# Kernel tuning notes

Hardware: AMD Instinct MI355X
Metric: run time of the kernel (lower is better)

## Reference

```python
import jax, jax.numpy as jnp
import numpy as np

PY_SIZES = [256, 64]
BASE = 256


def _resize_bilinear_ac(x, out):
    # NCHW bilinear resize, align_corners=True (matches F.interpolate(..., align_corners=True))
    def interp(x, axis, in_size):
        pos = jnp.arange(out, dtype=jnp.float32) * (in_size - 1) / (out - 1)
        lo = jnp.floor(pos).astype(jnp.int32)
        hi = jnp.minimum(lo + 1, in_size - 1)
        w = (pos - lo.astype(jnp.float32)).astype(x.dtype)
        shp = [1] * x.ndim
        shp[axis] = out
        w = w.reshape(shp)
        return jnp.take(x, lo, axis=axis) * (1 - w) + jnp.take(x, hi, axis=axis) * w
    x = interp(x, 2, x.shape[2])
    x = interp(x, 3, x.shape[3])
    return x


def _area_pool(x, f):
    # F.interpolate(mode='area') for integer downscale factor f == average pooling
    B, C, H, W = x.shape
    return x.reshape(B, C, H // f, f, W // f, f).mean(axis=(3, 5))


def _nearest_up_int(x, out):
    # F.interpolate(mode='nearest'): src = floor(dst * in/out)
    h = x.shape[2]
    idx = (jnp.arange(out) * h) // out
    return x[:, :, idx][:, :, :, idx]


def _buffers(B):
    grids, lin_ids, img_ids = [], [], []
    prev = 0
    for S in PY_SIZES:
        d = jnp.arange(S, dtype=jnp.float32) + 0.5
        gy, gx = jnp.meshgrid(d, d, indexing='ij')
        grids.append(jnp.broadcast_to(jnp.stack([gy, gx], -1)[None, None], (B, 1, S, S, 2)))
        lin_ids.append(jnp.arange(B * S * S, dtype=jnp.int32).reshape(B, 1, S, S) + prev)
        prev += B * S * S
        img_ids.append(jnp.broadcast_to(jnp.arange(B, dtype=jnp.float32)[:, None, None, None], (B, 1, S, S)))
    return grids, lin_ids, img_ids


def setup_inputs():
    key = jax.random.key(0)
    k1, k2 = jax.random.split(key)
    b_edges = (jax.random.uniform(k1, (64, 1, 512, 512)) < 0.08).astype(jnp.float32)
    sobel = jax.random.normal(k2, (64, 2, 512, 512), dtype=jnp.float32)
    return {"b_edges": b_edges, "sobel": sobel}


def reference(b_edges, sobel):
    B = b_edges.shape[0]
    grids, lin_ids, img_ids = _buffers(B)
    # resize post-Canny maps to base pyramid level
    e0 = jnp.clip(_resize_bilinear_ac(b_edges, BASE), 0, 1)
    s0 = _resize_bilinear_ac(sobel, BASE)
    py = [(e0, s0)]
    for S in PY_SIZES[1:]:
        f = BASE // S
        py.append((_area_pool(e0, f), _area_pool(s0, f)))
    p_lin, my_lin, centers, norms, sizes, imgid = [], [], [], [], [], []
    for i, (e, s) in enumerate(py):
        S = e.shape[2]
        idx = jnp.nonzero((e != 0).reshape(-1))[0]  # stream compaction of edge pixels
        if i + 1 < len(py):
            pl = _nearest_up_int(lin_ids[i + 1], S).reshape(-1)[idx]
        else:
            pl = lin_ids[i].reshape(-1)[idx]
        rat = BASE / S
        p_lin.append(pl)
        my_lin.append(lin_ids[i].reshape(-1)[idx])
        centers.append(grids[i].reshape(-1, 2)[idx] * rat)
        norms.append(jnp.transpose(s, (0, 2, 3, 1)).reshape(-1, 2)[idx])
        sizes.append(jnp.full(idx.shape, rat, dtype=jnp.float32))
        imgid.append(img_ids[i].reshape(-1)[idx])
    p_lin = jnp.concatenate(p_lin)
    my_lin = jnp.concatenate(my_lin)
    centers = jnp.concatenate(centers)
    norms = jnp.concatenate(norms)
    sizes = jnp.concatenate(sizes)
    imgid = jnp.concatenate(imgid)
    # parent scatter: linid -> row of that string, then gather by parent linid
    rowids = jnp.arange(my_lin.shape[0], dtype=jnp.int32)
    table = jnp.zeros(int(p_lin.max()) + 1, dtype=jnp.int32).at[my_lin].set(rowids)
    p_rowids = table[p_lin]
    norms = norms / jnp.linalg.norm(norms, axis=1, keepdims=True)
    # cross([nx,ny,0],[0,0,1]) = (ny,-nx,0)
    rt = jnp.stack([norms[:, 1], -norms[:, 0]], -1) * (sizes[:, None] / 2)
    locs_lf = centers + rt
    locs_rt = centers - rt
    return locs_lf, locs_rt, norms, sizes, centers, imgid, p_rowids, my_lin
```

## Files before the change

### kernel.cpp

```cpp
#include <hip/hip_runtime.h>
#include <math.h>


typedef unsigned long long u64;
#define OFFSET1 4194304

__global__ __launch_bounds__(256) void prepE_kernel(const float* __restrict__ E,
                                                    unsigned short* __restrict__ pred16,
                                                    u64* __restrict__ mask1,
                                                    int* __restrict__ counts0,
                                                    int* __restrict__ counts1) {
    int lane = threadIdx.x & 63;
    int g = blockIdx.x * 4 + (threadIdx.x >> 6);
    int b = g >> 6, R = g & 63;

    const float* Ep = E + b * 262144 + (8 * R) * 512 + 8 * lane;
    float4 L[8], H[8];
    #pragma unroll
    for (int k = 0; k < 8; ++k) {
        L[k] = *(const float4*)(Ep + k * 512);
        H[k] = *(const float4*)(Ep + k * 512 + 4);
    }

    float wx[4], cwx[4];
    #pragma unroll
    for (int j = 0; j < 4; ++j) {
        int xi = 4 * lane + j;
        wx[j] = (float)(xi * 511) / 255.0f - (float)(8 * lane + 2 * j);
        cwx[j] = 1.0f - wx[j];
    }

    unsigned pred = 0;
    int rc = 0;
    #pragma unroll
    for (int r = 0; r < 4; ++r) {
        int y = 4 * R + r;
        float wy = (float)(y * 511) / 255.0f - (float)(2 * y);
        float cwy = 1.0f - wy;
        float4 lo = L[2 * r], loh = H[2 * r];
        float4 hi = L[2 * r + 1], hih = H[2 * r + 1];
        float e0 = (lo.x*cwy + hi.x*wy)*cwx[0] + (lo.y*cwy + hi.y*wy)*wx[0];
        float e1 = (lo.z*cwy + hi.z*wy)*cwx[1] + (lo.w*cwy + hi.w*wy)*wx[1];
        float e2 = (loh.x*cwy + hih.x*wy)*cwx[2] + (loh.y*cwy + hih.y*wy)*wx[2];
        float e3 = (loh.z*cwy + hih.z*wy)*cwx[3] + (loh.w*cwy + hih.w*wy)*wx[3];
        bool p0 = (e0 != 0.0f), p1 = (e1 != 0.0f), p2 = (e2 != 0.0f), p3 = (e3 != 0.0f);
        pred |= (p0?1u:0u) << (4*r+0);
        pred |= (p1?1u:0u) << (4*r+1);
        pred |= (p2?1u:0u) << (4*r+2);
        pred |= (p3?1u:0u) << (4*r+3);
        u64 b0 = __ballot(p0), b1 = __ballot(p1), b2 = __ballot(p2), b3 = __ballot(p3);
        rc += __popcll(b0) + __popcll(b1) + __popcll(b2) + __popcll(b3);
    }
    u64 m1 = __ballot(pred != 0);
    pred16[g * 64 + lane] = (unsigned short)pred;
    if (lane == 0) {
        counts0[g] = rc;
        counts1[g] = __popcll(m1);
        mask1[g] = m1;
    }
}

__global__ __launch_bounds__(1024) void scan_kernel(const int* __restrict__ counts0,
                                                    int* __restrict__ offs0,
                                                    const int* __restrict__ counts1,
                                                    int* __restrict__ offs1,
                                                    int* __restrict__ totals) {
    __shared__ int wsum[16];
    int tid = threadIdx.x, lane = tid & 63, wave = tid >> 6;

    int carry = 0;
    for (int base = 0; base < 4096; base += 1024) {
        int v = counts0[base + tid];
        int inc = v;
        #pragma unroll
        for (int d = 1; d < 64; d <<= 1) {
            int t = __shfl_up(inc, (unsigned)d, 64);
            if (lane >= d) inc += t;
        }
        if (lane == 63) wsum[wave] = inc;
        __syncthreads();
        int wbase = 0;
        for (int i = 0; i < wave; ++i) wbase += wsum[i];
        int tot = 0;
        #pragma unroll
        for (int i = 0; i < 16; ++i) tot += wsum[i];
        offs0[base + tid] = carry + wbase + inc - v;
        carry += tot;
        __syncthreads();
    }
    if (tid == 0) totals[0] = carry;

    int carry1 = 0;
    for (int base = 0; base < 4096; base += 1024) {
        int v = counts1[base + tid];
        int inc = v;
        #pragma unroll
        for (int d = 1; d < 64; d <<= 1) {
            int t = __shfl_up(inc, (unsigned)d, 64);
            if (lane >= d) inc += t;
        }
        if (lane == 63) wsum[wave] = inc;
        __syncthreads();
        int wbase = 0;
        for (int i = 0; i < wave; ++i) wbase += wsum[i];
        int tot = 0;
        #pragma unroll
        for (int i = 0; i < 16; ++i) tot += wsum[i];
        offs1[base + tid] = carry1 + wbase + inc - v;
        carry1 += tot;
        __syncthreads();
    }
    if (tid == 0) totals[1] = carry1;
}

__device__ __forceinline__ void write_row(float* __restrict__ out, int N, int row,
                                          float cy, float cx, float s0v, float s1v,
                                          float half, float sz, float imgid,
                                          float prow, float mylin) {
    float len = sqrtf(s0v * s0v + s1v * s1v);
    float n0 = s0v / len, n1 = s1v / len;
    float rt0 = n1 * half, rt1 = -n0 * half;
    ((float2*)out)[row]           = make_float2(cy + rt0, cx + rt1);
    ((float2*)(out + 2 * N))[row] = make_float2(cy - rt0, cx - rt1);
    ((float2*)(out + 4 * N))[row] = make_float2(n0, n1);
    out[6 * N + row] = sz;
    ((float2*)(out + 7 * N))[row] = make_float2(cy, cx);
    out[9 * N + row] = imgid;
    out[10 * N + row] = prow;
    out[11 * N + row] = mylin;
}

__global__ __launch_bounds__(256) void prepS_kernel(const float* __restrict__ S,
                                                    const unsigned short* __restrict__ pred16,
                                                    const u64* __restrict__ mask1,
                                                    const int* __restrict__ offs0,
                                                    const int* __restrict__ offs1,
                                                    const int* __restrict__ totals,
                                                    float* __restrict__ out, int N) {
    int lane = threadIdx.x & 63;
    int g = blockIdx.x * 4 + (threadIdx.x >> 6);
    int bimg = g >> 6, R = g & 63;

    u64 m1 = mask1[g];
    if (m1 == 0ull) return;
    unsigned pred = pred16[g * 64 + lane];
    int base0 = offs0[g];
    int prow = totals[0] + offs1[g] + __popcll(m1 & ((1ull << lane) - 1ull));

    float wx[4], cwx[4];
    #pragma unroll
    for (int j = 0; j < 4; ++j) {
        int xi = 4 * lane + j;
        wx[j] = (float)(xi * 511) / 255.0f - (float)(8 * lane + 2 * j);
        cwx[j] = 1.0f - wx[j];
    }

    const float* Sa = S + (size_t)(2 * bimg) * 262144 + (8 * R) * 512 + 8 * lane;
    const float* Sq = Sa + 262144;

    float acc0 = 0.0f, acc1 = 0.0f;
    int rc = 0;
    #pragma unroll
    for (int h = 0; h < 2; ++h) {
        float4 A[4], Ax[4], Q[4], Qx[4];
        #pragma unroll
        for (int k = 0; k < 4; ++k) {
            const float* pa = Sa + (4 * h + k) * 512;
            A[k]  = *(const float4*)pa;
            Ax[k] = *(const float4*)(pa + 4);
            const float* pq = Sq + (4 * h + k) * 512;
            Q[k]  = *(const float4*)pq;
            Qx[k] = *(const float4*)(pq + 4);
        }
        #pragma unroll
        for (int rr = 0; rr < 2; ++rr) {
            int r = 2 * h + rr;
            int y = 4 * R + r;
            float wy = (float)(y * 511) / 255.0f - (float)(2 * y);
            float cwy = 1.0f - wy;
            float4 lo = A[2*rr], loh = Ax[2*rr], hi = A[2*rr+1], hih = Ax[2*rr+1];
            float4 ql = Q[2*rr], qlh = Qx[2*rr], qh = Q[2*rr+1], qhh = Qx[2*rr+1];
            float va[4], vb[4];
            va[0] = (lo.x*cwy + hi.x*wy)*cwx[0] + (lo.y*cwy + hi.y*wy)*wx[0];
            va[1] = (lo.z*cwy + hi.z*wy)*cwx[1] + (lo.w*cwy + hi.w*wy)*wx[1];
            va[2] = (loh.x*cwy + hih.x*wy)*cwx[2] + (loh.y*cwy + hih.y*wy)*wx[2];
            va[3] = (loh.z*cwy + hih.z*wy)*cwx[3] + (loh.w*cwy + hih.w*wy)*wx[3];
            vb[0] = (ql.x*cwy + qh.x*wy)*cwx[0] + (ql.y*cwy + qh.y*wy)*wx[0];
            vb[1] = (ql.z*cwy + qh.z*wy)*cwx[1] + (ql.w*cwy + qh.w*wy)*wx[1];
            vb[2] = (qlh.x*cwy + qhh.x*wy)*cwx[2] + (qlh.y*cwy + qhh.y*wy)*wx[2];
            vb[3] = (qlh.z*cwy + qhh.z*wy)*cwx[3] + (qlh.w*cwy + qhh.w*wy)*wx[3];
            acc0 += va[0] + va[1] + va[2] + va[3];
            acc1 += vb[0] + vb[1] + vb[2] + vb[3];

            unsigned pr = (pred >> (4 * r)) & 0xF;
            u64 b0 = __ballot(pr & 1);
            u64 b1 = __ballot(pr & 2);
            u64 b2 = __ballot(pr & 4);
            u64 b3 = __ballot(pr & 8);
            u64 ltm = (1ull << lane) - 1ull;
            int pre = __popcll(b0 & ltm) + __popcll(b1 & ltm) +
                      __popcll(b2 & ltm) + __popcll(b3 & ltm);
            int rbase = base0 + rc + pre;
            int own = 0;
            #pragma unroll
            for (int j = 0; j < 4; ++j) {
                if (pr & (1u << j)) {
                    int row = rbase + own;
                    own++;
                    int x = 4 * lane + j;
                    float cy = (float)y + 0.5f, cx = (float)x + 0.5f;
                    write_row(out, N, row, cy, cx, va[j], vb[j], 0.5f, 1.0f,
                              (float)bimg, (float)prow,
                              (float)((bimg << 16) + (y << 8) + x));
                }
            }
            rc += __popcll(b0) + __popcll(b1) + __popcll(b2) + __popcll(b3);
        }
    }

    if (pred != 0) {
        float v0 = acc0 * (1.0f / 16.0f), v1 = acc1 * (1.0f / 16.0f);
        float cy = ((float)R + 0.5f) * 4.0f, cx = ((float)lane + 0.5f) * 4.0f;
        write_row(out, N, prow, cy, cx, v0, v1, 2.0f, 4.0f, (float)bimg,
                  (float)prow, (float)(OFFSET1 + g * 64 + lane));
    }
}

extern "C" void kernel_launch(void* const* d_in, const int* in_sizes, int n_in,
                              void* d_out, int out_size, void* d_ws, size_t ws_size,
                              hipStream_t stream) {
    const float* E = (const float*)d_in[0];
    const float* S = (const float*)d_in[1];
    float* out = (float*)d_out;
    int N = out_size / 12;

    char* ws = (char*)d_ws;
    int* counts0 = (int*)(ws + 0);
    int* offs0   = (int*)(ws + 16384);
    int* counts1 = (int*)(ws + 32768);
    int* offs1   = (int*)(ws + 49152);
    int* totals  = (int*)(ws + 65536);
    u64* mask1   = (u64*)(ws + 65600);
    unsigned short* pred16 = (unsigned short*)(ws + 98368);

    prepE_kernel<<<1024, 256, 0, stream>>>(E, pred16, mask1, counts0, counts1);
    scan_kernel<<<1, 1024, 0, stream>>>(counts0, offs0, counts1, offs1, totals);
    prepS_kernel<<<1024, 256, 0, stream>>>(S, pred16, mask1, offs0, offs1,
                                           totals, out, N);
}
```

Measured before the change: 75.86 us.

## Split sobel resize kernel into half-row waves plus a level-1 finish kernel

```diff
diff --git a/kernel.cpp b/kernel.cpp
--- a/kernel.cpp
+++ b/kernel.cpp
@@ -130,20 +130,22 @@
     out[11 * N + row] = mylin;
 }
 
-__global__ __launch_bounds__(256) void prepS_kernel(const float* __restrict__ S,
-                                                    const unsigned short* __restrict__ pred16,
-                                                    const u64* __restrict__ mask1,
-                                                    const int* __restrict__ offs0,
-                                                    const int* __restrict__ offs1,
-                                                    const int* __restrict__ totals,
-                                                    float* __restrict__ out, int N) {
-    int lane = threadIdx.x & 63;
-    int g = blockIdx.x * 4 + (threadIdx.x >> 6);
+__global__ __launch_bounds__(256) void prepSa_kernel(const float* __restrict__ S,
+                                                     const unsigned short* __restrict__ pred16,
+                                                     const u64* __restrict__ mask1,
+                                                     const int* __restrict__ offs0,
+                                                     const int* __restrict__ offs1,
+                                                     const int* __restrict__ totals,
+                                                     float2* __restrict__ part,
+                                                     float* __restrict__ out, int N) {
+    int tid = threadIdx.x;
+    int lane = tid & 63;
+    int gh = blockIdx.x * 4 + (tid >> 6);
+    int g = gh >> 1, h = gh & 1;
     int bimg = g >> 6, R = g & 63;
 
+    unsigned pred = pred16[g * 64 + lane];
     u64 m1 = mask1[g];
-    if (m1 == 0ull) return;
-    unsigned pred = pred16[g * 64 + lane];
     int base0 = offs0[g];
     int prow = totals[0] + offs1[g] + __popcll(m1 & ((1ull << lane) - 1ull));
 
@@ -155,75 +157,95 @@
         cwx[j] = 1.0f - wx[j];
     }
 
-    const float* Sa = S + (size_t)(2 * bimg) * 262144 + (8 * R) * 512 + 8 * lane;
+    const float* Sa = S + (size_t)(2 * bimg) * 262144 + (8 * R + 4 * h) * 512 + 8 * lane;
     const float* Sq = Sa + 262144;
+    float4 A[4], Ax[4], Q[4], Qx[4];
+    #pragma unroll
+    for (int k = 0; k < 4; ++k) {
+        A[k]  = *(const float4*)(Sa + k * 512);
+        Ax[k] = *(const float4*)(Sa + k * 512 + 4);
+        Q[k]  = *(const float4*)(Sq + k * 512);
+        Qx[k] = *(const float4*)(Sq + k * 512 + 4);
+    }
+
+    int rc = 0;
+    if (h) {
+        #pragma unroll
+        for (int r = 0; r < 2; ++r) {
+            unsigned pr = (pred >> (4 * r)) & 0xF;
+            rc += __popcll(__ballot((pr & 1) != 0)) + __popcll(__ballot((pr & 2) != 0)) +
+                  __popcll(__ballot((pr & 4) != 0)) + __popcll(__ballot((pr & 8) != 0));
+        }
+    }
 
     float acc0 = 0.0f, acc1 = 0.0f;
-    int rc = 0;
-    #pragma unroll
-    for (int h = 0; h < 2; ++h) {
-        float4 A[4], Ax[4], Q[4], Qx[4];
-        #pragma unroll
-        for (int k = 0; k < 4; ++k) {
-            const float* pa = Sa + (4 * h + k) * 512;
-            A[k]  = *(const float4*)pa;
-            Ax[k] = *(const float4*)(pa + 4);
-            const float* pq = Sq + (4 * h + k) * 512;
-            Q[k]  = *(const float4*)pq;
-            Qx[k] = *(const float4*)(pq + 4);
-        }
-        #pragma unroll
-        for (int rr = 0; rr < 2; ++rr) {
-            int r = 2 * h + rr;
-            int y = 4 * R + r;
-            float wy = (float)(y * 511) / 255.0f - (float)(2 * y);
-            float cwy = 1.0f - wy;
-            float4 lo = A[2*rr], loh = Ax[2*rr], hi = A[2*rr+1], hih = Ax[2*rr+1];
-            float4 ql = Q[2*rr], qlh = Qx[2*rr], qh = Q[2*rr+1], qhh = Qx[2*rr+1];
-            float va[4], vb[4];
-            va[0] = (lo.x*cwy + hi.x*wy)*cwx[0] + (lo.y*cwy + hi.y*wy)*wx[0];
-            va[1] = (lo.z*cwy + hi.z*wy)*cwx[1] + (lo.w*cwy + hi.w*wy)*wx[1];
-            va[2] = (loh.x*cwy + hih.x*wy)*cwx[2] + (loh.y*cwy + hih.y*wy)*wx[2];
-            va[3] = (loh.z*cwy + hih.z*wy)*cwx[3] + (loh.w*cwy + hih.w*wy)*wx[3];
-            vb[0] = (ql.x*cwy + qh.x*wy)*cwx[0] + (ql.y*cwy + qh.y*wy)*wx[0];
-            vb[1] = (ql.z*cwy + qh.z*wy)*cwx[1] + (ql.w*cwy + qh.w*wy)*wx[1];
-            vb[2] = (qlh.x*cwy + qhh.x*wy)*cwx[2] + (qlh.y*cwy + qhh.y*wy)*wx[2];
-            vb[3] = (qlh.z*cwy + qhh.z*wy)*cwx[3] + (qlh.w*cwy + qhh.w*wy)*wx[3];
-            acc0 += va[0] + va[1] + va[2] + va[3];
-            acc1 += vb[0] + vb[1] + vb[2] + vb[3];
-
-            unsigned pr = (pred >> (4 * r)) & 0xF;
-            u64 b0 = __ballot(pr & 1);
-            u64 b1 = __ballot(pr & 2);
-            u64 b2 = __ballot(pr & 4);
-            u64 b3 = __ballot(pr & 8);
-            u64 ltm = (1ull << lane) - 1ull;
-            int pre = __popcll(b0 & ltm) + __popcll(b1 & ltm) +
-                      __popcll(b2 & ltm) + __popcll(b3 & ltm);
-            int rbase = base0 + rc + pre;
-            int own = 0;
-            #pragma unroll
-            for (int j = 0; j < 4; ++j) {
-                if (pr & (1u << j)) {
-                    int row = rbase + own;
-                    own++;
-                    int x = 4 * lane + j;
-                    float cy = (float)y + 0.5f, cx = (float)x + 0.5f;
-                    write_row(out, N, row, cy, cx, va[j], vb[j], 0.5f, 1.0f,
-                              (float)bimg, (float)prow,
-                              (float)((bimg << 16) + (y << 8) + x));
-                }
+    #pragma unroll
+    for (int rr = 0; rr < 2; ++rr) {
+        int r = 2 * h + rr;
+        int y = 4 * R + r;
+        float wy = (float)(y * 511) / 255.0f - (float)(2 * y);
+        float cwy = 1.0f - wy;
+        float4 lo = A[2*rr], loh = Ax[2*rr], hi = A[2*rr+1], hih = Ax[2*rr+1];
+        float4 ql = Q[2*rr], qlh = Qx[2*rr], qh = Q[2*rr+1], qhh = Qx[2*rr+1];
+        float va[4], vb[4];
+        va[0] = (lo.x*cwy + hi.x*wy)*cwx[0] + (lo.y*cwy + hi.y*wy)*wx[0];
+        va[1] = (lo.z*cwy + hi.z*wy)*cwx[1] + (lo.w*cwy + hi.w*wy)*wx[1];
+        va[2] = (loh.x*cwy + hih.x*wy)*cwx[2] + (loh.y*cwy + hih.y*wy)*wx[2];
+        va[3] = (loh.z*cwy + hih.z*wy)*cwx[3] + (loh.w*cwy + hih.w*wy)*wx[3];
+        vb[0] = (ql.x*cwy + qh.x*wy)*cwx[0] + (ql.y*cwy + qh.y*wy)*wx[0];
+        vb[1] = (ql.z*cwy + qh.z*wy)*cwx[1] + (ql.w*cwy + qh.w*wy)*wx[1];
+        vb[2] = (qlh.x*cwy + qhh.x*wy)*cwx[2] + (qlh.y*cwy + qhh.y*wy)*wx[2];
+        vb[3] = (qlh.z*cwy + qhh.z*wy)*cwx[3] + (qlh.w*cwy + qhh.w*wy)*wx[3];
+        acc0 += va[0] + va[1] + va[2] + va[3];
+        acc1 += vb[0] + vb[1] + vb[2] + vb[3];
+
+        unsigned pr = (pred >> (4 * r)) & 0xF;
+        u64 b0 = __ballot((pr & 1) != 0);
+        u64 b1 = __ballot((pr & 2) != 0);
+        u64 b2 = __ballot((pr & 4) != 0);
+        u64 b3 = __ballot((pr & 8) != 0);
+        u64 ltm = (1ull << lane) - 1ull;
+        int pre = __popcll(b0 & ltm) + __popcll(b1 & ltm) +
+                  __popcll(b2 & ltm) + __popcll(b3 & ltm);
+        int rbase = base0 + rc + pre;
+        int own = 0;
+        #pragma unroll
+        for (int j = 0; j < 4; ++j) {
+            if (pr & (1u << j)) {
+                int row = rbase + own;
+                own++;
+                int x = 4 * lane + j;
+                float cy = (float)y + 0.5f, cx = (float)x + 0.5f;
+                write_row(out, N, row, cy, cx, va[j], vb[j], 0.5f, 1.0f,
+                          (float)bimg, (float)prow,
+                          (float)((bimg << 16) + (y << 8) + x));
             }
-            rc += __popcll(b0) + __popcll(b1) + __popcll(b2) + __popcll(b3);
-        }
-    }
-
-    if (pred != 0) {
-        float v0 = acc0 * (1.0f / 16.0f), v1 = acc1 * (1.0f / 16.0f);
-        float cy = ((float)R + 0.5f) * 4.0f, cx = ((float)lane + 0.5f) * 4.0f;
-        write_row(out, N, prow, cy, cx, v0, v1, 2.0f, 4.0f, (float)bimg,
-                  (float)prow, (float)(OFFSET1 + g * 64 + lane));
-    }
+        }
+        rc += __popcll(b0) + __popcll(b1) + __popcll(b2) + __popcll(b3);
+    }
+
+    part[gh * 64 + lane] = make_float2(acc0, acc1);
+}
+
+__global__ __launch_bounds__(256) void finish1_kernel(const float2* __restrict__ part,
+                                                      const u64* __restrict__ mask1,
+                                                      const int* __restrict__ offs1,
+                                                      const int* __restrict__ totals,
+                                                      float* __restrict__ out, int N) {
+    int tid = threadIdx.x, lane = tid & 63;
+    int g = blockIdx.x * 4 + (tid >> 6);
+    u64 m1 = mask1[g];
+    if (m1 == 0ull) return;
+    float2 p0 = part[(2 * g) * 64 + lane];
+    float2 p1 = part[(2 * g + 1) * 64 + lane];
+    if (!((m1 >> lane) & 1ull)) return;
+    int prow = totals[0] + offs1[g] + __popcll(m1 & ((1ull << lane) - 1ull));
+    float v0 = (p0.x + p1.x) * (1.0f / 16.0f);
+    float v1 = (p0.y + p1.y) * (1.0f / 16.0f);
+    int bimg = g >> 6, R = g & 63;
+    float cy = ((float)R + 0.5f) * 4.0f, cx = ((float)lane + 0.5f) * 4.0f;
+    write_row(out, N, prow, cy, cx, v0, v1, 2.0f, 4.0f, (float)bimg,
+              (float)prow, (float)(OFFSET1 + g * 64 + lane));
 }
 
 extern "C" void kernel_launch(void* const* d_in, const int* in_sizes, int n_in,
@@ -242,9 +264,11 @@
     int* totals  = (int*)(ws + 65536);
     u64* mask1   = (u64*)(ws + 65600);
     unsigned short* pred16 = (unsigned short*)(ws + 98368);
+    float2* part = (float2*)(ws + 622656);
 
     prepE_kernel<<<1024, 256, 0, stream>>>(E, pred16, mask1, counts0, counts1);
     scan_kernel<<<1, 1024, 0, stream>>>(counts0, offs0, counts1, offs1, totals);
-    prepS_kernel<<<1024, 256, 0, stream>>>(S, pred16, mask1, offs0, offs1,
-                                           totals, out, N);
-}
+    prepSa_kernel<<<2048, 256, 0, stream>>>(S, pred16, mask1, offs0, offs1,
+                                            totals, part, out, N);
+    finish1_kernel<<<1024, 256, 0, stream>>>(part, mask1, offs1, totals, out, N);
+}
```

Result: no change. 76.25 us (+0.5%).

## Split output writing into compact payload plus coalesced SoA expand kernel

Applied to the files above, without the earlier changes.

```diff
diff --git a/kernel.cpp b/kernel.cpp
--- a/kernel.cpp
+++ b/kernel.cpp
@@ -113,37 +113,19 @@
     if (tid == 0) totals[1] = carry1;
 }
 
-__device__ __forceinline__ void write_row(float* __restrict__ out, int N, int row,
-                                          float cy, float cx, float s0v, float s1v,
-                                          float half, float sz, float imgid,
-                                          float prow, float mylin) {
-    float len = sqrtf(s0v * s0v + s1v * s1v);
-    float n0 = s0v / len, n1 = s1v / len;
-    float rt0 = n1 * half, rt1 = -n0 * half;
-    ((float2*)out)[row]           = make_float2(cy + rt0, cx + rt1);
-    ((float2*)(out + 2 * N))[row] = make_float2(cy - rt0, cx - rt1);
-    ((float2*)(out + 4 * N))[row] = make_float2(n0, n1);
-    out[6 * N + row] = sz;
-    ((float2*)(out + 7 * N))[row] = make_float2(cy, cx);
-    out[9 * N + row] = imgid;
-    out[10 * N + row] = prow;
-    out[11 * N + row] = mylin;
-}
-
-__global__ __launch_bounds__(256) void prepS_kernel(const float* __restrict__ S,
-                                                    const unsigned short* __restrict__ pred16,
-                                                    const u64* __restrict__ mask1,
-                                                    const int* __restrict__ offs0,
-                                                    const int* __restrict__ offs1,
-                                                    const int* __restrict__ totals,
-                                                    float* __restrict__ out, int N) {
+__global__ __launch_bounds__(256) void sval_kernel(const float* __restrict__ S,
+                                                   const unsigned short* __restrict__ pred16,
+                                                   const u64* __restrict__ mask1,
+                                                   const int* __restrict__ offs0,
+                                                   const int* __restrict__ offs1,
+                                                   const int* __restrict__ totals,
+                                                   int4* __restrict__ payload) {
     int lane = threadIdx.x & 63;
     int g = blockIdx.x * 4 + (threadIdx.x >> 6);
     int bimg = g >> 6, R = g & 63;
 
+    unsigned pred = pred16[g * 64 + lane];
     u64 m1 = mask1[g];
-    if (m1 == 0ull) return;
-    unsigned pred = pred16[g * 64 + lane];
     int base0 = offs0[g];
     int prow = totals[0] + offs1[g] + __popcll(m1 & ((1ull << lane) - 1ull));
 
@@ -155,22 +137,20 @@
         cwx[j] = 1.0f - wx[j];
     }
 
-    const float* Sa = S + (size_t)(2 * bimg) * 262144 + (8 * R) * 512 + 8 * lane;
-    const float* Sq = Sa + 262144;
-
+    const float* Sa0 = S + (size_t)(2 * bimg) * 262144 + (8 * R) * 512 + 8 * lane;
     float acc0 = 0.0f, acc1 = 0.0f;
     int rc = 0;
     #pragma unroll
     for (int h = 0; h < 2; ++h) {
+        const float* Sa = Sa0 + (4 * h) * 512;
+        const float* Sq = Sa + 262144;
         float4 A[4], Ax[4], Q[4], Qx[4];
         #pragma unroll
         for (int k = 0; k < 4; ++k) {
-            const float* pa = Sa + (4 * h + k) * 512;
-            A[k]  = *(const float4*)pa;
-            Ax[k] = *(const float4*)(pa + 4);
-            const float* pq = Sq + (4 * h + k) * 512;
-            Q[k]  = *(const float4*)pq;
-            Qx[k] = *(const float4*)(pq + 4);
+            A[k]  = *(const float4*)(Sa + k * 512);
+            Ax[k] = *(const float4*)(Sa + k * 512 + 4);
+            Q[k]  = *(const float4*)(Sq + k * 512);
+            Qx[k] = *(const float4*)(Sq + k * 512 + 4);
         }
         #pragma unroll
         for (int rr = 0; rr < 2; ++rr) {
@@ -193,10 +173,10 @@
             acc1 += vb[0] + vb[1] + vb[2] + vb[3];
 
             unsigned pr = (pred >> (4 * r)) & 0xF;
-            u64 b0 = __ballot(pr & 1);
-            u64 b1 = __ballot(pr & 2);
-            u64 b2 = __ballot(pr & 4);
-            u64 b3 = __ballot(pr & 8);
+            u64 b0 = __ballot((pr & 1) != 0);
+            u64 b1 = __ballot((pr & 2) != 0);
+            u64 b2 = __ballot((pr & 4) != 0);
+            u64 b3 = __ballot((pr & 8) != 0);
             u64 ltm = (1ull << lane) - 1ull;
             int pre = __popcll(b0 & ltm) + __popcll(b1 & ltm) +
                       __popcll(b2 & ltm) + __popcll(b3 & ltm);
@@ -205,13 +185,10 @@
             #pragma unroll
             for (int j = 0; j < 4; ++j) {
                 if (pr & (1u << j)) {
-                    int row = rbase + own;
+                    payload[rbase + own] =
+                        make_int4(__float_as_int(va[j]), __float_as_int(vb[j]),
+                                  (bimg << 16) | (y << 8) | (4 * lane + j), prow);
                     own++;
-                    int x = 4 * lane + j;
-                    float cy = (float)y + 0.5f, cx = (float)x + 0.5f;
-                    write_row(out, N, row, cy, cx, va[j], vb[j], 0.5f, 1.0f,
-                              (float)bimg, (float)prow,
-                              (float)((bimg << 16) + (y << 8) + x));
                 }
             }
             rc += __popcll(b0) + __popcll(b1) + __popcll(b2) + __popcll(b3);
@@ -219,10 +196,88 @@
     }
 
     if (pred != 0) {
-        float v0 = acc0 * (1.0f / 16.0f), v1 = acc1 * (1.0f / 16.0f);
-        float cy = ((float)R + 0.5f) * 4.0f, cx = ((float)lane + 0.5f) * 4.0f;
-        write_row(out, N, prow, cy, cx, v0, v1, 2.0f, 4.0f, (float)bimg,
-                  (float)prow, (float)(OFFSET1 + g * 64 + lane));
+        payload[prow] = make_int4(__float_as_int(acc0 * (1.0f / 16.0f)),
+                                  __float_as_int(acc1 * (1.0f / 16.0f)),
+                                  OFFSET1 + g * 64 + lane, prow);
+    }
+}
+
+__global__ __launch_bounds__(256) void expand_kernel(const int4* __restrict__ payload,
+                                                     float* __restrict__ out, int N) {
+    __shared__ float rowv[12][256];
+    int t = threadIdx.x;
+    int base = blockIdx.x * 256;
+    int cnt = N - base; if (cnt > 256) cnt = 256;
+
+    if (t < cnt) {
+        int4 p = payload[base + t];
+        float v0 = __int_as_float(p.x), v1 = __int_as_float(p.y);
+        int pid = p.z, prw = p.w;
+        float cy, cx, half, sz, mylin;
+        int b;
+        if (pid >= OFFSET1) {
+            int lin = pid - OFFSET1;
+            b = lin >> 12;
+            int R = (lin >> 6) & 63, X = lin & 63;
+            cy = ((float)R + 0.5f) * 4.0f; cx = ((float)X + 0.5f) * 4.0f;
+            half = 2.0f; sz = 4.0f; mylin = (float)pid;
+        } else {
+            b = pid >> 16;
+            int y = (pid >> 8) & 255, x = pid & 255;
+            cy = (float)y + 0.5f; cx = (float)x + 0.5f;
+            half = 0.5f; sz = 1.0f; mylin = (float)pid;
+        }
+        float len = sqrtf(v0 * v0 + v1 * v1);
+        float n0 = v0 / len, n1 = v1 / len;
+        float rt0 = n1 * half, rt1 = -n0 * half;
+        rowv[0][t] = cy + rt0;  rowv[1][t] = cx + rt1;
+        rowv[2][t] = cy - rt0;  rowv[3][t] = cx - rt1;
+        rowv[4][t] = n0;        rowv[5][t] = n1;
+        rowv[6][t] = sz;
+        rowv[7][t] = cy;        rowv[8][t] = cx;
+        rowv[9][t] = (float)b;
+        rowv[10][t] = (float)prw;
+        rowv[11][t] = mylin;
+    }
+    __syncthreads();
+
+    const int mult[8] = {0, 2, 4, 6, 7, 9, 10, 11};
+    const int wid[8]  = {2, 2, 2, 1, 2, 1, 1, 1};
+    const int col[8]  = {0, 2, 4, 6, 7, 9, 10, 11};
+    #pragma unroll 1
+    for (int s = 0; s < 8; ++s) {
+        int w = wid[s];
+        float* P = out + (size_t)mult[s] * N + (size_t)w * base;
+        int total = w * cnt;
+        int head = (int)((16 - ((uintptr_t)P & 15)) & 15) >> 2;
+        if (head > total) head = total;
+        if (t < head) {
+            int r = (w == 2) ? (t >> 1) : t;
+            int c = (w == 2) ? (t & 1) : 0;
+            P[t] = rowv[col[s] + c][r];
+        }
+        int nb4 = (total - head) >> 2;
+        #pragma unroll 1
+        for (int k = t; k < nb4; k += 256) {
+            int f = head + 4 * k;
+            float4 v;
+            #pragma unroll
+            for (int u = 0; u < 4; ++u) {
+                int ff = f + u;
+                int r = (w == 2) ? (ff >> 1) : ff;
+                int c = (w == 2) ? (ff & 1) : 0;
+                (&v.x)[u] = rowv[col[s] + c][r];
+            }
+            *(float4*)(P + f) = v;
+        }
+        int done = head + 4 * nb4;
+        int rem = total - done;
+        if (t < rem) {
+            int ff = done + t;
+            int r = (w == 2) ? (ff >> 1) : ff;
+            int c = (w == 2) ? (ff & 1) : 0;
+            P[ff] = rowv[col[s] + c][r];
+        }
     }
 }
 
@@ -236,15 +291,17 @@
 
     char* ws = (char*)d_ws;
     int* counts0 = (int*)(ws + 0);
-    int* offs0   = (int*)(ws + 16384);
-    int* counts1 = (int*)(ws + 32768);
+    int* counts1 = (int*)(ws + 16384);
+    int* offs0   = (int*)(ws + 32768);
     int* offs1   = (int*)(ws + 49152);
     int* totals  = (int*)(ws + 65536);
     u64* mask1   = (u64*)(ws + 65600);
     unsigned short* pred16 = (unsigned short*)(ws + 98368);
+    int4* payload = (int4*)(ws + 622656);
 
     prepE_kernel<<<1024, 256, 0, stream>>>(E, pred16, mask1, counts0, counts1);
     scan_kernel<<<1, 1024, 0, stream>>>(counts0, offs0, counts1, offs1, totals);
-    prepS_kernel<<<1024, 256, 0, stream>>>(S, pred16, mask1, offs0, offs1,
-                                           totals, out, N);
-}
+    sval_kernel<<<1024, 256, 0, stream>>>(S, pred16, mask1, offs0, offs1,
+                                          totals, payload);
+    expand_kernel<<<(N + 255) / 256, 256, 0, stream>>>(payload, out, N);
+}
```

After: 82.07 us. 1.08x slower.

## Fuse prefix scan into prepE via last-block-done atomic counter

Applied to the files above, without the earlier changes.

```diff
diff --git a/kernel.cpp b/kernel.cpp
--- a/kernel.cpp
+++ b/kernel.cpp
@@ -4,14 +4,26 @@
 
 typedef unsigned long long u64;
 #define OFFSET1 4194304
+
+__device__ __forceinline__ int aload(const int* p) {
+    return __hip_atomic_load(p, __ATOMIC_RELAXED, __HIP_MEMORY_SCOPE_AGENT);
+}
+__device__ __forceinline__ void astore(int* p, int v) {
+    __hip_atomic_store(p, v, __ATOMIC_RELAXED, __HIP_MEMORY_SCOPE_AGENT);
+}
 
 __global__ __launch_bounds__(256) void prepE_kernel(const float* __restrict__ E,
                                                     unsigned short* __restrict__ pred16,
                                                     u64* __restrict__ mask1,
                                                     int* __restrict__ counts0,
-                                                    int* __restrict__ counts1) {
-    int lane = threadIdx.x & 63;
-    int g = blockIdx.x * 4 + (threadIdx.x >> 6);
+                                                    int* __restrict__ counts1,
+                                                    int* __restrict__ offs0,
+                                                    int* __restrict__ offs1,
+                                                    int* __restrict__ totals,
+                                                    int* __restrict__ syn) {
+    int tid = threadIdx.x;
+    int lane = tid & 63, wave = tid >> 6;
+    int g = blockIdx.x * 4 + wave;
     int b = g >> 6, R = g & 63;
 
     const float* Ep = E + b * 262144 + (8 * R) * 512 + 8 * lane;
@@ -54,23 +66,26 @@
     u64 m1 = __ballot(pred != 0);
     pred16[g * 64 + lane] = (unsigned short)pred;
     if (lane == 0) {
-        counts0[g] = rc;
-        counts1[g] = __popcll(m1);
+        astore(&counts0[g], rc);
+        astore(&counts1[g], __popcll(m1));
         mask1[g] = m1;
     }
-}
-
-__global__ __launch_bounds__(1024) void scan_kernel(const int* __restrict__ counts0,
-                                                    int* __restrict__ offs0,
-                                                    const int* __restrict__ counts1,
-                                                    int* __restrict__ offs1,
-                                                    int* __restrict__ totals) {
-    __shared__ int wsum[16];
-    int tid = threadIdx.x, lane = tid & 63, wave = tid >> 6;
-
+
+    __syncthreads();
+    __shared__ int is_scanner;
+    if (tid == 0) {
+        __threadfence();
+        int old = __hip_atomic_fetch_add(&syn[0], 1, __ATOMIC_ACQ_REL,
+                                         __HIP_MEMORY_SCOPE_AGENT);
+        is_scanner = (old == (int)gridDim.x - 1);
+    }
+    __syncthreads();
+    if (!is_scanner) return;
+
+    __shared__ int wsum[4];
     int carry = 0;
-    for (int base = 0; base < 4096; base += 1024) {
-        int v = counts0[base + tid];
+    for (int base = 0; base < 4096; base += 256) {
+        int v = aload(&counts0[base + tid]);
         int inc = v;
         #pragma unroll
         for (int d = 1; d < 64; d <<= 1) {
@@ -81,18 +96,15 @@
         __syncthreads();
         int wbase = 0;
         for (int i = 0; i < wave; ++i) wbase += wsum[i];
-        int tot = 0;
-        #pragma unroll
-        for (int i = 0; i < 16; ++i) tot += wsum[i];
-        offs0[base + tid] = carry + wbase + inc - v;
+        int tot = wsum[0] + wsum[1] + wsum[2] + wsum[3];
+        astore(&offs0[base + tid], carry + wbase + inc - v);
         carry += tot;
         __syncthreads();
     }
-    if (tid == 0) totals[0] = carry;
-
+    if (tid == 0) astore(&totals[0], carry);
     int carry1 = 0;
-    for (int base = 0; base < 4096; base += 1024) {
-        int v = counts1[base + tid];
+    for (int base = 0; base < 4096; base += 256) {
+        int v = aload(&counts1[base + tid]);
         int inc = v;
         #pragma unroll
         for (int d = 1; d < 64; d <<= 1) {
@@ -103,14 +115,12 @@
         __syncthreads();
         int wbase = 0;
         for (int i = 0; i < wave; ++i) wbase += wsum[i];
-        int tot = 0;
-        #pragma unroll
-        for (int i = 0; i < 16; ++i) tot += wsum[i];
-        offs1[base + tid] = carry1 + wbase + inc - v;
+        int tot = wsum[0] + wsum[1] + wsum[2] + wsum[3];
+        astore(&offs1[base + tid], carry1 + wbase + inc - v);
         carry1 += tot;
         __syncthreads();
     }
-    if (tid == 0) totals[1] = carry1;
+    if (tid == 0) astore(&totals[1], carry1);
 }
 
 __device__ __forceinline__ void write_row(float* __restrict__ out, int N, int row,
@@ -144,8 +154,9 @@
     u64 m1 = mask1[g];
     if (m1 == 0ull) return;
     unsigned pred = pred16[g * 64 + lane];
-    int base0 = offs0[g];
-    int prow = totals[0] + offs1[g] + __popcll(m1 & ((1ull << lane) - 1ull));
+    int base0 = aload(&offs0[g]);
+    int prow = aload(&totals[0]) + aload(&offs1[g]) +
+               __popcll(m1 & ((1ull << lane) - 1ull));
 
     float wx[4], cwx[4];
     #pragma unroll
@@ -193,10 +204,10 @@
             acc1 += vb[0] + vb[1] + vb[2] + vb[3];
 
             unsigned pr = (pred >> (4 * r)) & 0xF;
-            u64 b0 = __ballot(pr & 1);
-            u64 b1 = __ballot(pr & 2);
-            u64 b2 = __ballot(pr & 4);
-            u64 b3 = __ballot(pr & 8);
+            u64 b0 = __ballot((pr & 1) != 0);
+            u64 b1 = __ballot((pr & 2) != 0);
+            u64 b2 = __ballot((pr & 4) != 0);
+            u64 b3 = __ballot((pr & 8) != 0);
             u64 ltm = (1ull << lane) - 1ull;
             int pre = __popcll(b0 & ltm) + __popcll(b1 & ltm) +
                       __popcll(b2 & ltm) + __popcll(b3 & ltm);
@@ -240,11 +251,13 @@
     int* counts1 = (int*)(ws + 32768);
     int* offs1   = (int*)(ws + 49152);
     int* totals  = (int*)(ws + 65536);
+    int* syn     = (int*)(ws + 65544);
     u64* mask1   = (u64*)(ws + 65600);
     unsigned short* pred16 = (unsigned short*)(ws + 98368);
 
-    prepE_kernel<<<1024, 256, 0, stream>>>(E, pred16, mask1, counts0, counts1);
-    scan_kernel<<<1, 1024, 0, stream>>>(counts0, offs0, counts1, offs1, totals);
+    hipMemsetAsync(syn, 0, sizeof(int), stream);
+    prepE_kernel<<<1024, 256, 0, stream>>>(E, pred16, mask1, counts0, counts1,
+                                           offs0, offs1, totals, syn);
     prepS_kernel<<<1024, 256, 0, stream>>>(S, pred16, mask1, offs0, offs1,
                                            totals, out, N);
 }
```

Result: slower. 152.7 us (+101.3%).
